# Optimization experiments

Hardware: AMD Instinct MI355X
Metric: run time of the kernel (lower is better)

Reference implementation:

```python
import jax, jax.numpy as jnp
import numpy as np

B, T, C = 1, 2048, 1024
H = 16
HD = C // H
BLOCK = 2048
NEG = float('-inf')

def setup_inputs() -> dict:
    key = jax.random.key(0)
    ks = jax.random.split(key, 6)
    x = jax.random.normal(ks[0], (B, T, C), dtype=jnp.float32)
    cumulative_scores = jax.random.normal(ks[1], (B, T), dtype=jnp.float32) * 0.1
    padding_mask = jnp.ones((B, T), dtype=jnp.float32)
    token_index = jax.random.randint(ks[2], (B, T), 0, BLOCK).astype(jnp.int64)
    w_attn = jax.random.normal(ks[3], (C, 3 * C), dtype=jnp.float32) * (1.0 / np.sqrt(C))
    b_attn = jnp.zeros((3 * C,), dtype=jnp.float32)
    w_proj = jax.random.normal(ks[4], (C, C), dtype=jnp.float32) * (1.0 / np.sqrt(C))
    b_proj = jnp.zeros((C,), dtype=jnp.float32)
    return dict(x=x, cumulative_scores=cumulative_scores, padding_mask=padding_mask,
                token_index=token_index, w_attn=w_attn, b_attn=b_attn,
                w_proj=w_proj, b_proj=b_proj)

def _rotate_half(z):
    z1, z2 = z[..., : z.shape[-1] // 2], z[..., z.shape[-1] // 2 :]
    return jnp.concatenate((-z2, z1), axis=-1)

def reference(x, cumulative_scores, padding_mask, token_index, w_attn, b_attn, w_proj, b_proj):
    # fused QKV projection
    qkv = x @ w_attn + b_attn                      # (B,T,3C)
    q, k, v = jnp.split(qkv, 3, axis=2)
    q = q.reshape(B, T, H, HD).transpose(0, 2, 1, 3)  # (B,H,T,HD)
    k = k.reshape(B, T, H, HD).transpose(0, 2, 1, 3)
    v = v.reshape(B, T, H, HD).transpose(0, 2, 1, 3)

    # dynamic per-token RoPE positions: global token counts (original scatter
    # broadcasts indices over batch, so counts are global across all batches)
    cnt = jnp.zeros((BLOCK,), jnp.float32).at[token_index.reshape(-1)].add(1.0)
    per_tok = (1.0 / (cnt + 1e-10))[token_index]       # (B,T)
    partial = jnp.cumsum(per_tok, axis=-1)             # (B,T) fractional positions

    inv_freq = 1.0 / (10000.0 ** (jnp.arange(0, HD, 2, dtype=jnp.float32) / HD))
    freqs = partial[..., None] * inv_freq              # (B,T,HD/2)
    emb = jnp.concatenate((freqs, freqs), axis=-1)     # (B,T,HD)
    cos = jnp.cos(emb)[:, None]                        # (B,1,T,HD)
    sin = jnp.sin(emb)[:, None]
    q = q * cos + _rotate_half(q) * sin
    k = k * cos + _rotate_half(k) * sin

    # 'fork' plan: overwrite last channel
    q = q.at[..., -1].set(1.0)
    k = k.at[..., -1].set(jnp.broadcast_to(cumulative_scores[:, None, :], (B, H, T)))

    # additive causal + padding mask (B,T,T)
    causal = jnp.where(jnp.tril(jnp.ones((T, T), jnp.bool_)), 0.0, NEG)
    pm = jnp.take_along_axis(padding_mask, token_index, axis=1)     # (B,T)
    outer = pm[:, :, None] * pm[:, None, :]
    pad_add = jnp.where(outer.astype(jnp.bool_), 0.0, NEG)
    mask = causal[None, :, :] + pad_add                              # (B,T,T)

    # scale v by exp(cumulative_scores)
    v = v * jnp.exp(cumulative_scores)[:, None, :, None]

    scores = jnp.einsum('bhqd,bhkd->bhqk', q, k) / np.sqrt(HD) + mask[:, None]
    probs = jax.nn.softmax(scores, axis=-1)
    y = jnp.einsum('bhqk,bhkd->bhqd', probs, v)        # (B,H,T,HD)
    y = y.transpose(0, 2, 1, 3).reshape(B, T, C)
    return y @ w_proj + b_proj
```

## Files before the change

### kernel.cpp

```cpp
#include <hip/hip_runtime.h>
#include <math.h>

#define T 2048
#define C 1024
#define H 16
#define HD 64
#define N3 (3*C)
#define NBLOCK 2048

typedef __attribute__((ext_vector_type(8))) short bf16x8;
typedef __attribute__((ext_vector_type(4))) float f32x4;

#define MFMA16(a, b, c) __builtin_amdgcn_mfma_f32_16x16x32_bf16((a), (b), (c), 0, 0, 0)

__device__ inline short f2bf(float f) {
    unsigned u; __builtin_memcpy(&u, &f, 4);
    unsigned r = (u + 0x7fffu + ((u >> 16) & 1u)) >> 16;
    return (short)r;
}
__device__ inline float bf2f(short s) {
    unsigned u = ((unsigned)(unsigned short)s) << 16;
    float f; __builtin_memcpy(&f, &u, 4);
    return f;
}

__device__ inline void gload_lds16(const void* g, void* l) {
    __builtin_amdgcn_global_load_lds((const __attribute__((address_space(1))) unsigned int*)g,
                                     (__attribute__((address_space(3))) unsigned int*)l,
                                     16, 0, 0);
}

__global__ __launch_bounds__(256) void pre_kernel(const float* __restrict__ x,
                                                  const float* __restrict__ w_attn,
                                                  const float* __restrict__ w_proj,
                                                  const int* __restrict__ tok,
                                                  const float* __restrict__ padmask,
                                                  short* __restrict__ xb,
                                                  short* __restrict__ wabT,
                                                  short* __restrict__ wpbT,
                                                  float* __restrict__ partial,
                                                  float* __restrict__ pm_tok) {
    int bid = blockIdx.x;
    int tid = threadIdx.x;
    if (bid == 3072) {
        __shared__ float cntS[NBLOCK];
        __shared__ float sums[256];
        #pragma unroll
        for (int j = 0; j < 8; ++j) cntS[tid * 8 + j] = 0.0f;
        __syncthreads();
        int tk[8];
        #pragma unroll
        for (int j = 0; j < 8; ++j) {
            tk[j] = tok[tid * 8 + j];
            atomicAdd(&cntS[tk[j]], 1.0f);
        }
        __syncthreads();
        float vals[8];
        float s = 0.0f;
        #pragma unroll
        for (int j = 0; j < 8; ++j) {
            s += 1.0f / (cntS[tk[j]] + 1e-10f);
            vals[j] = s;
            pm_tok[tid * 8 + j] = padmask[tk[j]];
        }
        sums[tid] = s;
        __syncthreads();
        for (int off = 1; off < 256; off <<= 1) {
            float v = (tid >= off) ? sums[tid - off] : 0.0f;
            __syncthreads();
            sums[tid] += v;
            __syncthreads();
        }
        float offset = (tid > 0) ? sums[tid - 1] : 0.0f;
        #pragma unroll
        for (int j = 0; j < 8; ++j) partial[tid * 8 + j] = offset + vals[j];
        return;
    }
    if (bid < 2048) {
        int i = bid * 1024 + tid * 4;
        float4 v = *(const float4*)(x + i);
        short4 o;
        o.x = f2bf(v.x); o.y = f2bf(v.y); o.z = f2bf(v.z); o.w = f2bf(v.w);
        *(short4*)(xb + i) = o;
        return;
    }
    __shared__ float S[64][65];
    const float* in; short* out; int Kd, Nd, bx, by;
    if (bid < 2816) {
        int b = bid - 2048;
        bx = b % 48; by = b / 48;
        in = w_attn; out = wabT; Kd = C; Nd = N3;
    } else {
        int b = bid - 2816;
        bx = b % 16; by = b / 16;
        in = w_proj; out = wpbT; Kd = C; Nd = C;
    }
    int n0 = bx * 64, k0 = by * 64;
    #pragma unroll
    for (int i = 0; i < 16; ++i) {
        int lin = tid + i * 256;
        int r = lin >> 6, c = lin & 63;
        S[r][c] = in[(size_t)(k0 + r) * Nd + n0 + c];
    }
    __syncthreads();
    #pragma unroll
    for (int i = 0; i < 16; ++i) {
        int lin = tid + i * 256;
        int rn = lin >> 6, ck = lin & 63;
        out[(size_t)(n0 + rn) * Kd + k0 + ck] = f2bf(S[ck][rn]);
    }
}

template <int OUT_BF16, int EPI>
__global__ __launch_bounds__(256) void gemm_bt64(const short* __restrict__ A,
                                                 const short* __restrict__ Bt,
                                                 const float* __restrict__ bias,
                                                 void* __restrict__ Cout,
                                                 int M, int N, int K,
                                                 const float* __restrict__ partial,
                                                 const float* __restrict__ cumsc,
                                                 const float* __restrict__ pm_tok,
                                                 short* __restrict__ vbT) {
    __shared__ alignas(16) short As[64 * 32];
    __shared__ alignas(16) short Bs[128 * 32];
    int tid = threadIdx.x;
    int m0 = blockIdx.y * 64, n0 = blockIdx.x * 128;
    int w = tid >> 6, l = tid & 63;
    int wm = (w >> 1) * 32, wn = (w & 1) * 64;
    int lq = l & 15, g = l >> 4;
    int prow = l >> 2, pcol = (l & 3) * 8;
    f32x4 acc[2][4] = {};
    for (int k0 = 0; k0 < K; k0 += 32) {
        {
            int rowA = w * 16 + prow;
            gload_lds16(A + (size_t)(m0 + rowA) * K + k0 + pcol, As + w * 512);
            #pragma unroll
            for (int i = 0; i < 2; ++i) {
                int c = w * 2 + i;
                int row = c * 16 + prow;
                gload_lds16(Bt + (size_t)(n0 + row) * K + k0 + pcol, Bs + c * 512);
            }
        }
        __syncthreads();
        bf16x8 af[2], bfr[4];
        #pragma unroll
        for (int f = 0; f < 2; ++f)
            af[f] = *(const bf16x8*)(As + (wm + f * 16 + lq) * 32 + g * 8);
        #pragma unroll
        for (int j = 0; j < 4; ++j)
            bfr[j] = *(const bf16x8*)(Bs + (wn + j * 16 + lq) * 32 + g * 8);
        #pragma unroll
        for (int fi = 0; fi < 2; ++fi)
            #pragma unroll
            for (int fj = 0; fj < 4; ++fj)
                acc[fi][fj] = MFMA16(af[fi], bfr[fj], acc[fi][fj]);
        __syncthreads();
    }

    if (EPI == 0) {
        #pragma unroll
        for (int fi = 0; fi < 2; ++fi)
            #pragma unroll
            for (int fj = 0; fj < 4; ++fj)
                #pragma unroll
                for (int r = 0; r < 4; ++r) {
                    int m = m0 + wm + fi * 16 + g * 4 + r;
                    int n = n0 + wn + fj * 16 + lq;
                    float v = acc[fi][fj][r] + bias[n];
                    if (OUT_BF16) ((short*)Cout)[(size_t)m * N + n] = f2bf(v);
                    else          ((float*)Cout)[(size_t)m * N + n] = v;
                }
    } else {
        short* Cb = (short*)Cout;
        int cb = n0 + wn;
        int section = cb >> 10;
        float b0 = bias[cb + lq],      b1 = bias[cb + 16 + lq];
        float b2 = bias[cb + 32 + lq], b3 = bias[cb + 48 + lq];
        if (section < 2) {
            bool isQ = (section == 0);
            float inv0 = exp2f(-(float)lq * (13.287712379549449f / 32.0f));
            float inv1 = exp2f(-(float)(lq + 16) * (13.287712379549449f / 32.0f));
            #pragma unroll
            for (int fi = 0; fi < 2; ++fi)
                #pragma unroll
                for (int r = 0; r < 4; ++r) {
                    int trow = m0 + wm + fi * 16 + g * 4 + r;
                    float pt = partial[trow];
                    float sn0, cs0, sn1, cs1;
                    __sincosf(pt * inv0, &sn0, &cs0);
                    __sincosf(pt * inv1, &sn1, &cs1);
                    float a0 = acc[fi][0][r] + b0;
                    float a1 = acc[fi][1][r] + b1;
                    float a2 = acc[fi][2][r] + b2;
                    float a3 = acc[fi][3][r] + b3;
                    float lo0 = a0 * cs0 - a2 * sn0;
                    float hi0 = a2 * cs0 + a0 * sn0;
                    float lo1 = a1 * cs1 - a3 * sn1;
                    float hi1 = a3 * cs1 + a1 * sn1;
                    if (lq == 15) {
                        float pm = pm_tok[trow];
                        hi1 = isQ ? ((pm != 0.0f) ? 1.0f : 0.0f)
                                  : ((pm != 0.0f) ? cumsc[trow] : -1e20f);
                    }
                    size_t base = (size_t)trow * N3 + cb;
                    Cb[base + lq]      = f2bf(lo0);
                    Cb[base + 16 + lq] = f2bf(lo1);
                    Cb[base + 32 + lq] = f2bf(hi0);
                    Cb[base + 48 + lq] = f2bf(hi1);
                }
        } else {
            int h = (cb - 2 * C) >> 6;
            #pragma unroll
            for (int fi = 0; fi < 2; ++fi) {
                int tb = m0 + wm + fi * 16 + g * 4;
                float ef[4];
                #pragma unroll
                for (int r = 0; r < 4; ++r) ef[r] = __expf(cumsc[tb + r]);
                #pragma unroll
                for (int fj = 0; fj < 4; ++fj) {
                    int d = fj * 16 + lq;
                    float bv = (fj == 0) ? b0 : (fj == 1) ? b1 : (fj == 2) ? b2 : b3;
                    short4 o;
                    o.x = f2bf((acc[fi][fj][0] + bv) * ef[0]);
                    o.y = f2bf((acc[fi][fj][1] + bv) * ef[1]);
                    o.z = f2bf((acc[fi][fj][2] + bv) * ef[2]);
                    o.w = f2bf((acc[fi][fj][3] + bv) * ef[3]);
                    *(short4*)(vbT + (size_t)(h * 64 + d) * T + tb) = o;
                }
            }
        }
    }
}

__global__ __launch_bounds__(256) void attn_flash(const short* __restrict__ qkvb,
                                                  const short* __restrict__ vbT,
                                                  short* __restrict__ yb) {
    __shared__ alignas(16) short Kt[2][64 * 64];
    __shared__ alignas(16) short Vt[2][64 * 64];
    __shared__ alignas(16) short Ps[4][16][72];

    int b = blockIdx.x;
    int h, qt;
    if (b < 256) { h = b & 15; qt = 31 - (b >> 4); }
    else         { int c2 = b - 256; h = c2 & 15; qt = c2 >> 4; }
    int tid = threadIdx.x;
    int w = tid >> 6, l = tid & 63;
    int lq = l & 15, g = l >> 4;
    int qrl = w * 16 + lq;

    const short* qbase = qkvb + (size_t)(qt * 64 + qrl) * N3 + h * 64;
    bf16x8 qf0 = *(const bf16x8*)(qbase + g * 8);
    bf16x8 qf1 = *(const bf16x8*)(qbase + 32 + g * 8);

    f32x4 accO[4] = {};
    float lsum = 0.0f;

    int srow = tid >> 3, scol = (tid & 7) * 8;
    const short* kgb = qkvb + C + h * 64 + scol;
    const short* vgb = vbT + (size_t)(h * 64) * T + scol;
    int wb0 = srow * 128 + ((scol * 2) ^ ((srow & 7) << 4));
    int wb1 = (srow + 32) * 128 + ((scol * 2) ^ ((srow & 7) << 4));

    auto do_tile = [&](int cur, bool masked) {
        const char* Kc = (const char*)Kt[cur];
        const char* Vc = (const char*)Vt[cur];
        f32x4 s[4] = {};
        __builtin_amdgcn_s_setprio(1);
        #pragma unroll
        for (int f = 0; f < 4; ++f) {
            int row = f * 16 + lq;
            const char* kr_ = Kc + row * 128;
            int sw = (row & 7) << 4;
            bf16x8 a0 = *(const bf16x8*)(kr_ + ((g * 16) ^ sw));
            bf16x8 a1 = *(const bf16x8*)(kr_ + ((64 + g * 16) ^ sw));
            s[f] = MFMA16(a0, qf0, s[f]);
            s[f] = MFMA16(a1, qf1, s[f]);
        }
        __builtin_amdgcn_s_setprio(0);
        float p[16];
        #pragma unroll
        for (int f = 0; f < 4; ++f)
            #pragma unroll
            for (int r = 0; r < 4; ++r) {
                float sv = s[f][r] * 0.125f;
                if (masked) {
                    int kl = f * 16 + g * 4 + r;
                    sv = (kl > qrl) ? -INFINITY : sv;
                }
                float pv = __expf(sv);
                p[f * 4 + r] = pv;
                lsum += pv;
            }
        #pragma unroll
        for (int f = 0; f < 4; ++f) {
            unsigned u0, u1;
            asm("v_cvt_pk_bf16_f32 %0, %1, %2" : "=v"(u0) : "v"(p[f * 4 + 0]), "v"(p[f * 4 + 1]));
            asm("v_cvt_pk_bf16_f32 %0, %1, %2" : "=v"(u1) : "v"(p[f * 4 + 2]), "v"(p[f * 4 + 3]));
            uint2 uu; uu.x = u0; uu.y = u1;
            *(uint2*)&Ps[w][lq][f * 16 + g * 4] = uu;
        }
        __builtin_amdgcn_s_setprio(1);
        #pragma unroll
        for (int kh = 0; kh < 2; ++kh) {
            bf16x8 pa = *(const bf16x8*)&Ps[w][lq][kh * 32 + g * 8];
            #pragma unroll
            for (int f = 0; f < 4; ++f) {
                int vrow = f * 16 + lq;
                const char* vr_ = Vc + vrow * 128;
                bf16x8 vb = *(const bf16x8*)(vr_ + (((kh * 32 + g * 8) * 2) ^ ((vrow & 7) << 4)));
                accO[f] = MFMA16(pa, vb, accO[f]);
            }
        }
        __builtin_amdgcn_s_setprio(0);
    };

    uint4 kr0 = *(const uint4*)(kgb + (size_t)srow * N3);
    uint4 kr1 = *(const uint4*)(kgb + (size_t)(srow + 32) * N3);
    uint4 vr0 = *(const uint4*)(vgb + (size_t)srow * T);
    uint4 vr1 = *(const uint4*)(vgb + (size_t)(srow + 32) * T);
    *(uint4*)((char*)Kt[0] + wb0) = kr0;
    *(uint4*)((char*)Kt[0] + wb1) = kr1;
    *(uint4*)((char*)Vt[0] + wb0) = vr0;
    *(uint4*)((char*)Vt[0] + wb1) = vr1;
    __syncthreads();

    for (int t = 0; t < qt; ++t) {
        int kn = (t + 1) * 64;
        kr0 = *(const uint4*)(kgb + (size_t)(kn + srow) * N3);
        kr1 = *(const uint4*)(kgb + (size_t)(kn + srow + 32) * N3);
        vr0 = *(const uint4*)(vgb + (size_t)srow * T + kn);
        vr1 = *(const uint4*)(vgb + (size_t)(srow + 32) * T + kn);

        do_tile(t & 1, false);

        int nxt = (t & 1) ^ 1;
        *(uint4*)((char*)Kt[nxt] + wb0) = kr0;
        *(uint4*)((char*)Kt[nxt] + wb1) = kr1;
        *(uint4*)((char*)Vt[nxt] + wb0) = vr0;
        *(uint4*)((char*)Vt[nxt] + wb1) = vr1;
        __syncthreads();
    }
    do_tile(qt & 1, true);

    lsum += __shfl_xor(lsum, 16);
    lsum += __shfl_xor(lsum, 32);
    float linv_own = 1.0f / lsum;
    float li[4];
    #pragma unroll
    for (int r = 0; r < 4; ++r) li[r] = __shfl(linv_own, g * 4 + r);

    #pragma unroll
    for (int f = 0; f < 4; ++f)
        #pragma unroll
        for (int r = 0; r < 4; ++r) {
            int trow = qt * 64 + w * 16 + g * 4 + r;
            yb[(size_t)trow * C + h * 64 + f * 16 + lq] = f2bf(accO[f][r] * li[r]);
        }
}

extern "C" void kernel_launch(void* const* d_in, const int* in_sizes, int n_in,
                              void* d_out, int out_size, void* d_ws, size_t ws_size,
                              hipStream_t stream) {
    const float* x       = (const float*)d_in[0];
    const float* cumsc   = (const float*)d_in[1];
    const float* padmask = (const float*)d_in[2];
    const int*   tok     = (const int*)d_in[3];
    const float* w_attn  = (const float*)d_in[4];
    const float* b_attn  = (const float*)d_in[5];
    const float* w_proj  = (const float*)d_in[6];
    const float* b_proj  = (const float*)d_in[7];
    float* out = (float*)d_out;

    float* part   = (float*)d_ws;
    float* pm_tok = part + 2048;
    short* xb     = (short*)(pm_tok + 2048);
    short* wabT   = xb + (size_t)T * C;
    short* wpbT   = wabT + (size_t)N3 * C;
    short* qkvb   = wpbT + (size_t)C * C;
    short* vbT    = qkvb + (size_t)T * N3;
    short* yb     = vbT + (size_t)C * T;

    pre_kernel<<<3073, 256, 0, stream>>>(x, w_attn, w_proj, tok, padmask,
                                         xb, wabT, wpbT, part, pm_tok);
    gemm_bt64<1, 1><<<dim3(N3 / 128, T / 64), 256, 0, stream>>>(
        xb, wabT, b_attn, qkvb, T, N3, C, part, cumsc, pm_tok, vbT);
    attn_flash<<<512, 256, 0, stream>>>(qkvb, vbT, yb);
    gemm_bt64<0, 0><<<dim3(C / 128, T / 64), 256, 0, stream>>>(
        yb, wpbT, b_proj, out, T, C, C, nullptr, nullptr, nullptr, nullptr);
}
```

Before: 88.53 us.

## Move w_proj transpose-convert into attention launch and swizzle P scratch in LDS

The w_proj fp32-to-bf16 transpose moves out of the pre-kernel and into 256 extra blocks of the attention kernel. There it can fill SMs that sit idle in the attention tail, and the pre-kernel launch gets shorter. It also swaps the padded P staging buffer for an XOR-swizzled layout to avoid LDS bank conflicts. The extra blocks reuse the K tile LDS as scratch and use vectorized loads and stores, but they may compete with attention blocks for CUs.

New measurement: 88.71 us. No clear change (+0.2%).

```diff
diff --git a/kernel.cpp b/kernel.cpp
--- a/kernel.cpp
+++ b/kernel.cpp
@@ -32,17 +32,15 @@
 
 __global__ __launch_bounds__(256) void pre_kernel(const float* __restrict__ x,
                                                   const float* __restrict__ w_attn,
-                                                  const float* __restrict__ w_proj,
                                                   const int* __restrict__ tok,
                                                   const float* __restrict__ padmask,
                                                   short* __restrict__ xb,
                                                   short* __restrict__ wabT,
-                                                  short* __restrict__ wpbT,
                                                   float* __restrict__ partial,
                                                   float* __restrict__ pm_tok) {
     int bid = blockIdx.x;
     int tid = threadIdx.x;
-    if (bid == 3072) {
+    if (bid == 2816) {
         __shared__ float cntS[NBLOCK];
         __shared__ float sums[256];
         #pragma unroll
@@ -85,29 +83,21 @@
         return;
     }
     __shared__ float S[64][65];
-    const float* in; short* out; int Kd, Nd, bx, by;
-    if (bid < 2816) {
-        int b = bid - 2048;
-        bx = b % 48; by = b / 48;
-        in = w_attn; out = wabT; Kd = C; Nd = N3;
-    } else {
-        int b = bid - 2816;
-        bx = b % 16; by = b / 16;
-        in = w_proj; out = wpbT; Kd = C; Nd = C;
-    }
+    int b = bid - 2048;
+    int bx = b % 48, by = b / 48;
     int n0 = bx * 64, k0 = by * 64;
     #pragma unroll
     for (int i = 0; i < 16; ++i) {
         int lin = tid + i * 256;
         int r = lin >> 6, c = lin & 63;
-        S[r][c] = in[(size_t)(k0 + r) * Nd + n0 + c];
+        S[r][c] = w_attn[(size_t)(k0 + r) * N3 + n0 + c];
     }
     __syncthreads();
     #pragma unroll
     for (int i = 0; i < 16; ++i) {
         int lin = tid + i * 256;
         int rn = lin >> 6, ck = lin & 63;
-        out[(size_t)(n0 + rn) * Kd + k0 + ck] = f2bf(S[ck][rn]);
+        wabT[(size_t)(n0 + rn) * C + k0 + ck] = f2bf(S[ck][rn]);
     }
 }
 
@@ -234,19 +224,53 @@
 
 __global__ __launch_bounds__(256) void attn_flash(const short* __restrict__ qkvb,
                                                   const short* __restrict__ vbT,
-                                                  short* __restrict__ yb) {
+                                                  short* __restrict__ yb,
+                                                  const float* __restrict__ w_proj,
+                                                  short* __restrict__ wpbT) {
     __shared__ alignas(16) short Kt[2][64 * 64];
     __shared__ alignas(16) short Vt[2][64 * 64];
-    __shared__ alignas(16) short Ps[4][16][72];
+    __shared__ alignas(16) short Ps[4][16 * 64];
 
     int b = blockIdx.x;
+    int tid = threadIdx.x;
+
+    if (b >= 512) {
+        int bb = b - 512;
+        int bx = bb & 15, by = bb >> 4;
+        int n0 = bx * 64, k0 = by * 64;
+        short (*S)[72] = (short(*)[72])Kt;
+        #pragma unroll
+        for (int e = 0; e < 2; ++e) {
+            int s = tid * 2 + e;
+            int r = s >> 3, c8 = (s & 7) * 8;
+            float4 v0 = *(const float4*)(w_proj + (size_t)(k0 + r) * C + n0 + c8);
+            float4 v1 = *(const float4*)(w_proj + (size_t)(k0 + r) * C + n0 + c8 + 4);
+            bf16x8 o;
+            o[0] = f2bf(v0.x); o[1] = f2bf(v0.y); o[2] = f2bf(v0.z); o[3] = f2bf(v0.w);
+            o[4] = f2bf(v1.x); o[5] = f2bf(v1.y); o[6] = f2bf(v1.z); o[7] = f2bf(v1.w);
+            *(bf16x8*)&S[r][c8] = o;
+        }
+        __syncthreads();
+        #pragma unroll
+        for (int e = 0; e < 2; ++e) {
+            int s = tid * 2 + e;
+            int rn = s >> 3, k8 = (s & 7) * 8;
+            bf16x8 o;
+            #pragma unroll
+            for (int i = 0; i < 8; ++i) o[i] = S[k8 + i][rn];
+            *(bf16x8*)(wpbT + (size_t)(n0 + rn) * C + k0 + k8) = o;
+        }
+        return;
+    }
+
     int h, qt;
     if (b < 256) { h = b & 15; qt = 31 - (b >> 4); }
     else         { int c2 = b - 256; h = c2 & 15; qt = c2 >> 4; }
-    int tid = threadIdx.x;
     int w = tid >> 6, l = tid & 63;
     int lq = l & 15, g = l >> 4;
     int qrl = w * 16 + lq;
+    char* psBase = (char*)Ps + w * 2048 + lq * 128;
+    int psSw = (lq & 7) << 4;
 
     const short* qbase = qkvb + (size_t)(qt * 64 + qrl) * N3 + h * 64;
     bf16x8 qf0 = *(const bf16x8*)(qbase + g * 8);
@@ -297,12 +321,12 @@
             asm("v_cvt_pk_bf16_f32 %0, %1, %2" : "=v"(u0) : "v"(p[f * 4 + 0]), "v"(p[f * 4 + 1]));
             asm("v_cvt_pk_bf16_f32 %0, %1, %2" : "=v"(u1) : "v"(p[f * 4 + 2]), "v"(p[f * 4 + 3]));
             uint2 uu; uu.x = u0; uu.y = u1;
-            *(uint2*)&Ps[w][lq][f * 16 + g * 4] = uu;
+            *(uint2*)(psBase + ((f * 32 + g * 8) ^ psSw)) = uu;
         }
         __builtin_amdgcn_s_setprio(1);
         #pragma unroll
         for (int kh = 0; kh < 2; ++kh) {
-            bf16x8 pa = *(const bf16x8*)&Ps[w][lq][kh * 32 + g * 8];
+            bf16x8 pa = *(const bf16x8*)(psBase + ((kh * 64 + g * 16) ^ psSw));
             #pragma unroll
             for (int f = 0; f < 4; ++f) {
                 int vrow = f * 16 + lq;
@@ -380,11 +404,11 @@
     short* vbT    = qkvb + (size_t)T * N3;
     short* yb     = vbT + (size_t)C * T;
 
-    pre_kernel<<<3073, 256, 0, stream>>>(x, w_attn, w_proj, tok, padmask,
-                                         xb, wabT, wpbT, part, pm_tok);
+    pre_kernel<<<2817, 256, 0, stream>>>(x, w_attn, tok, padmask,
+                                         xb, wabT, part, pm_tok);
     gemm_bt64<1, 1><<<dim3(N3 / 128, T / 64), 256, 0, stream>>>(
         xb, wabT, b_attn, qkvb, T, N3, C, part, cumsc, pm_tok, vbT);
-    attn_flash<<<512, 256, 0, stream>>>(qkvb, vbT, yb);
+    attn_flash<<<768, 256, 0, stream>>>(qkvb, vbT, yb, w_proj, wpbT);
     gemm_bt64<0, 0><<<dim3(C / 128, T / 64), 256, 0, stream>>>(
         yb, wpbT, b_proj, out, T, C, C, nullptr, nullptr, nullptr, nullptr);
 }
```

## Fuse output projection into attention kernel via per-row-tile completion flags

Applied to the files above, without the earlier changes.

Appends 256 extra blocks to the attention launch. Each one spin-waits on an atomic counter until all 16 heads of its 64-row query tile have written their output, then computes that tile of the output projection GEMM. This removes a separate kernel launch and lets the projection overlap with the tail of attention. It adds a memset, fences and atomics, and depends on the attention blocks being scheduled before the waiting projection blocks. Spinning blocks can occupy compute units, and the simpler unpipelined projection loop may be slower than the standalone GEMM.

Measured after the change: 199.5 us. +125.3%, slower.

```diff
diff --git a/kernel.cpp b/kernel.cpp
--- a/kernel.cpp
+++ b/kernel.cpp
@@ -234,16 +234,78 @@
 
 __global__ __launch_bounds__(256) void attn_flash(const short* __restrict__ qkvb,
                                                   const short* __restrict__ vbT,
-                                                  short* __restrict__ yb) {
+                                                  short* __restrict__ yb,
+                                                  const short* __restrict__ wpbT,
+                                                  const float* __restrict__ b_proj,
+                                                  float* __restrict__ outp,
+                                                  int* __restrict__ flags) {
     __shared__ alignas(16) short Kt[2][64 * 64];
     __shared__ alignas(16) short Vt[2][64 * 64];
     __shared__ alignas(16) short Ps[4][16][72];
 
     int b = blockIdx.x;
+    int tid = threadIdx.x;
+
+    if (b >= 512) {
+        int bb = b - 512;
+        int bx = bb & 7, by = bb >> 3;
+        int m0 = by * 64, n0 = bx * 128;
+        if (tid == 0) {
+            int it = 0;
+            while (atomicAdd(&flags[by], 0) < 16 && it < (1 << 21)) {
+                __builtin_amdgcn_s_sleep(2);
+                ++it;
+            }
+        }
+        __syncthreads();
+        __threadfence();
+        short* Asp = &Kt[0][0];
+        short* Bsp = &Kt[1][0];
+        int w = tid >> 6, l = tid & 63;
+        int wm = (w >> 1) * 32, wn = (w & 1) * 64;
+        int lq = l & 15, g = l >> 4;
+        int prow = l >> 2, pcol = (l & 3) * 8;
+        f32x4 acc[2][4] = {};
+        for (int k0 = 0; k0 < C; k0 += 32) {
+            int rowA = w * 16 + prow;
+            gload_lds16(yb + (size_t)(m0 + rowA) * C + k0 + pcol, Asp + w * 512);
+            #pragma unroll
+            for (int i = 0; i < 2; ++i) {
+                int c = w * 2 + i;
+                int row = c * 16 + prow;
+                gload_lds16(wpbT + (size_t)(n0 + row) * C + k0 + pcol, Bsp + c * 512);
+            }
+            __syncthreads();
+            bf16x8 af[2], bfr[4];
+            #pragma unroll
+            for (int f = 0; f < 2; ++f)
+                af[f] = *(const bf16x8*)(Asp + (wm + f * 16 + lq) * 32 + g * 8);
+            #pragma unroll
+            for (int j = 0; j < 4; ++j)
+                bfr[j] = *(const bf16x8*)(Bsp + (wn + j * 16 + lq) * 32 + g * 8);
+            #pragma unroll
+            for (int fi = 0; fi < 2; ++fi)
+                #pragma unroll
+                for (int fj = 0; fj < 4; ++fj)
+                    acc[fi][fj] = MFMA16(af[fi], bfr[fj], acc[fi][fj]);
+            __syncthreads();
+        }
+        #pragma unroll
+        for (int fi = 0; fi < 2; ++fi)
+            #pragma unroll
+            for (int fj = 0; fj < 4; ++fj)
+                #pragma unroll
+                for (int r = 0; r < 4; ++r) {
+                    int m = m0 + wm + fi * 16 + g * 4 + r;
+                    int n = n0 + wn + fj * 16 + lq;
+                    outp[(size_t)m * C + n] = acc[fi][fj][r] + b_proj[n];
+                }
+        return;
+    }
+
     int h, qt;
     if (b < 256) { h = b & 15; qt = 31 - (b >> 4); }
     else         { int c2 = b - 256; h = c2 & 15; qt = c2 >> 4; }
-    int tid = threadIdx.x;
     int w = tid >> 6, l = tid & 63;
     int lq = l & 15, g = l >> 4;
     int qrl = w * 16 + lq;
@@ -356,6 +418,10 @@
             int trow = qt * 64 + w * 16 + g * 4 + r;
             yb[(size_t)trow * C + h * 64 + f * 16 + lq] = f2bf(accO[f][r] * li[r]);
         }
+
+    __threadfence();
+    __syncthreads();
+    if (tid == 0) atomicAdd(&flags[qt], 1);
 }
 
 extern "C" void kernel_launch(void* const* d_in, const int* in_sizes, int n_in,
@@ -373,7 +439,8 @@
 
     float* part   = (float*)d_ws;
     float* pm_tok = part + 2048;
-    short* xb     = (short*)(pm_tok + 2048);
+    int*   flags  = (int*)(pm_tok + 2048);
+    short* xb     = (short*)(flags + 2048);
     short* wabT   = xb + (size_t)T * C;
     short* wpbT   = wabT + (size_t)N3 * C;
     short* qkvb   = wpbT + (size_t)C * C;
@@ -382,9 +449,8 @@
 
     pre_kernel<<<3073, 256, 0, stream>>>(x, w_attn, w_proj, tok, padmask,
                                          xb, wabT, wpbT, part, pm_tok);
+    hipMemsetAsync(flags, 0, 32 * sizeof(int), stream);
     gemm_bt64<1, 1><<<dim3(N3 / 128, T / 64), 256, 0, stream>>>(
         xb, wabT, b_attn, qkvb, T, N3, C, part, cumsc, pm_tok, vbT);
-    attn_flash<<<512, 256, 0, stream>>>(qkvb, vbT, yb);
-    gemm_bt64<0, 0><<<dim3(C / 128, T / 64), 256, 0, stream>>>(
-        yb, wpbT, b_proj, out, T, C, C, nullptr, nullptr, nullptr, nullptr);
-}
+    attn_flash<<<768, 256, 0, stream>>>(qkvb, vbT, yb, wpbT, b_proj, out, flags);
+}
```
